# Performance work log

Hardware: AMD Instinct MI355X
Metric: run time of the kernel (lower is better)

## Reference

```python
import jax, jax.numpy as jnp
import numpy as np

N = 50000        # nodes
E = 800000       # edges
R = 8            # relations
G = 64           # g_dim
H1 = 64          # h1_dim
H2 = 32          # h2_dim (per-head for transformer, output for sage)
HEADS = 4
EPS = 1e-5       # BatchNorm eps


def setup_inputs() -> dict:
    key = jax.random.key(0)
    ks = jax.random.split(key, 16)
    def rn(k, shape, scale=0.05):
        return jax.random.normal(k, shape, dtype=jnp.float32) * scale
    return {
        "node_features": jax.random.normal(ks[0], (N, G), dtype=jnp.float32),
        "node_type": jax.random.randint(ks[1], (N,), 0, 3),
        "edge_index": jax.random.randint(ks[2], (2, E), 0, N),
        "edge_type": jax.random.randint(ks[3], (E,), 0, R),
        # RGCNConv params (per-relation weight + root weight + bias)
        "rgcn_w": rn(ks[4], (R, G, H1)),
        "rgcn_root": rn(ks[5], (G, H1)),
        "rgcn_bias": jnp.zeros((H1,), jnp.float32),
        "bn1_g": jnp.ones((H1,), jnp.float32),
        "bn1_b": jnp.zeros((H1,), jnp.float32),
        # TransformerConv params (q/k/v projections + skip)
        "wq": rn(ks[6], (H1, HEADS * H2)), "bq": jnp.zeros((HEADS * H2,), jnp.float32),
        "wk": rn(ks[7], (H1, HEADS * H2)), "bk": jnp.zeros((HEADS * H2,), jnp.float32),
        "wv": rn(ks[8], (H1, HEADS * H2)), "bv": jnp.zeros((HEADS * H2,), jnp.float32),
        "wskip": rn(ks[9], (H1, HEADS * H2)), "bskip": jnp.zeros((HEADS * H2,), jnp.float32),
        "bn2_g": jnp.ones((HEADS * H2,), jnp.float32),
        "bn2_b": jnp.zeros((HEADS * H2,), jnp.float32),
        # SAGEConv params (lin_l on aggregated neighbors has bias; lin_r on root has none)
        "sage_wl": rn(ks[10], (HEADS * H2, H2)), "sage_bl": jnp.zeros((H2,), jnp.float32),
        "sage_wr": rn(ks[11], (HEADS * H2, H2)),
        "bn3_g": jnp.ones((H2,), jnp.float32),
        "bn3_b": jnp.zeros((H2,), jnp.float32),
    }


def _bn(x, g, b):
    # BatchNorm1d in training mode: biased batch statistics over nodes
    m = x.mean(0)
    v = x.var(0)
    return g * (x - m) * jax.lax.rsqrt(v + EPS) + b


def _match(res, d):
    # F.pad(res, (0, d - c)): pads with zeros if d > c, truncates if d < c
    c = res.shape[1]
    if d > c:
        return jnp.pad(res, ((0, 0), (0, d - c)))
    return res[:, :d]


def _forward(node_features, rgcn_w, rgcn_root, rgcn_bias, bn1_g, bn1_b,
             wq, bq, wk, bk, wv, bv, wskip, bskip, bn2_g, bn2_b,
             sage_wl, sage_bl, sage_wr, bn3_g, bn3_b,
             edge_index, edge_type):
    src, dst = edge_index[0], edge_index[1]
    x = node_features
    residual = x

    # ---- RGCNConv: per-relation transform, per-relation mean aggregation, sum over relations ----
    xr = jnp.einsum('nf,rfh->nrh', x, rgcn_w)            # [N,R,H1]
    msg = xr[src, edge_type]                              # [E,H1]
    seg = dst * R + edge_type                             # segment per (node, relation)
    sums = jax.ops.segment_sum(msg, seg, num_segments=N * R)
    cnt = jax.ops.segment_sum(jnp.ones((E,), msg.dtype), seg, num_segments=N * R)
    agg = (sums / jnp.maximum(cnt, 1.0)[:, None]).reshape(N, R, H1).sum(1)
    h = agg + x @ rgcn_root + rgcn_bias
    h = jax.nn.leaky_relu(_bn(h, bn1_g, bn1_b))
    x = h + _match(residual, h.shape[1])
    residual = x

    # ---- TransformerConv: edge softmax attention, concat heads, + skip projection ----
    q = (x @ wq + bq).reshape(N, HEADS, H2)
    k = (x @ wk + bk).reshape(N, HEADS, H2)
    v = (x @ wv + bv).reshape(N, HEADS, H2)
    logits = (q[dst] * k[src]).sum(-1) / jnp.sqrt(jnp.float32(H2))  # [E,HEADS]
    mx = jax.ops.segment_max(logits, dst, num_segments=N)
    ex = jnp.exp(logits - mx[dst])
    den = jax.ops.segment_sum(ex, dst, num_segments=N)
    alpha = ex / jnp.maximum(den[dst], 1e-16)
    out = jax.ops.segment_sum(alpha[:, :, None] * v[src], dst, num_segments=N)
    h = out.reshape(N, HEADS * H2) + x @ wskip + bskip
    h = jax.nn.leaky_relu(_bn(h, bn2_g, bn2_b))
    x = h + _match(residual, h.shape[1])
    residual = x

    # ---- SAGEConv: mean neighbor aggregation + root transform ----
    nsum = jax.ops.segment_sum(x[src], dst, num_segments=N)
    ncnt = jax.ops.segment_sum(jnp.ones((E,), x.dtype), dst, num_segments=N)
    nmean = nsum / jnp.maximum(ncnt, 1.0)[:, None]
    h = nmean @ sage_wl + sage_bl + x @ sage_wr
    h = jax.nn.leaky_relu(_bn(h, bn3_g, bn3_b))
    return h + _match(residual, h.shape[1])


def reference(node_features, node_type, edge_index, edge_type,
              rgcn_w, rgcn_root, rgcn_bias, bn1_g, bn1_b,
              wq, bq, wk, bk, wv, bv, wskip, bskip, bn2_g, bn2_b,
              sage_wl, sage_bl, sage_wr, bn3_g, bn3_b):
    # node_type is unused by the original forward
    return _forward(node_features, rgcn_w, rgcn_root, rgcn_bias, bn1_g, bn1_b,
                    wq, bq, wk, bk, wv, bv, wskip, bskip, bn2_g, bn2_b,
                    sage_wl, sage_bl, sage_wr, bn3_g, bn3_b,
                    edge_index, edge_type)
```

## Files before the change

### kernel.cpp

```cpp
#include <hip/hip_runtime.h>
#include <stdint.h>

#define NN 50000
#define NE 800000
#define NR (NN*8)
#define SCAN_BS 512
#define NB2 782
#define INV_N (1.0f/50000.0f)
#define BN_EPS 1e-5f

typedef unsigned short ushort_t;
typedef unsigned char uchar_t;
typedef short bf16x8 __attribute__((ext_vector_type(8)));
typedef float f32x4 __attribute__((ext_vector_type(4)));
typedef float f32x2 __attribute__((ext_vector_type(2)));

__device__ __forceinline__ ushort_t f2bf(float f){
    unsigned int u = __float_as_uint(f);
    u += 0x7FFFu + ((u >> 16) & 1u);
    return (ushort_t)(u >> 16);
}
__device__ __forceinline__ float bf2f(ushort_t h){ return __uint_as_float(((unsigned int)h) << 16); }
__device__ __forceinline__ float bflo(unsigned int u){ return __uint_as_float(u << 16); }
__device__ __forceinline__ float bfhi(unsigned int u){ return __uint_as_float(u & 0xFFFF0000u); }

__device__ __forceinline__ unsigned int f4_to_fp8(float a, float b, float c, float d){
    int v = __builtin_amdgcn_cvt_pk_fp8_f32(a, b, 0, false);
    v = __builtin_amdgcn_cvt_pk_fp8_f32(c, d, v, true);
    return (unsigned int)v;
}
__device__ __forceinline__ void fp8_to_f4(unsigned int u, float& a, float& b, float& c, float& d){
    f32x2 lo = __builtin_amdgcn_cvt_pk_f32_fp8(u, false);
    f32x2 hi = __builtin_amdgcn_cvt_pk_f32_fp8(u, true);
    a = lo.x; b = lo.y; c = hi.x; d = hi.y;
}

__global__ void k_deg(const int* __restrict__ ei, const int* __restrict__ et,
                      int* __restrict__ deg, uint2* __restrict__ sr){
    int e = blockIdx.x*256 + threadIdx.x;
    if (e < NE){
        int seg = ei[NE + e]*8 + et[e];
        int rank = atomicAdd(&deg[seg], 1);
        uint2 o; o.x = (unsigned)seg; o.y = (unsigned)rank;
        sr[e] = o;
    }
}

__global__ void k_scan1(const int* __restrict__ deg, int* __restrict__ tmp, int* __restrict__ bsum){
    __shared__ int s[SCAN_BS];
    int t = threadIdx.x;
    int i = blockIdx.x*SCAN_BS + t;
    s[t] = (i < NR) ? deg[i] : 0;
    __syncthreads();
    for (int off = 1; off < SCAN_BS; off <<= 1){
        int add = (t >= off) ? s[t-off] : 0;
        __syncthreads();
        s[t] += add;
        __syncthreads();
    }
    if (i < NR) tmp[i] = s[t];
    if (t == SCAN_BS-1) bsum[blockIdx.x] = s[t];
}

__global__ void k_scan2(int* __restrict__ bsum){
    __shared__ int s[NB2];
    int t = threadIdx.x;
    if (t < NB2) s[t] = bsum[t];
    __syncthreads();
    if (t == 0){
        int acc = 0;
        for (int i = 0; i < NB2; ++i){ acc += s[i]; s[i] = acc; }
    }
    __syncthreads();
    if (t < NB2) bsum[t] = s[t];
}

__global__ void k_scan3(const int* __restrict__ tmp, const int* __restrict__ bsum, int* __restrict__ rs){
    int i = blockIdx.x*256 + threadIdx.x;
    if (i < NR){
        int b = i >> 9;
        int off = (b > 0) ? bsum[b-1] : 0;
        rs[i+1] = tmp[i] + off;
        if (i == 0) rs[0] = 0;
    }
}

__global__ void k_fill(const int* __restrict__ ei, const uint2* __restrict__ sr,
                       const int* __restrict__ rs, int* __restrict__ csr){
    int e = blockIdx.x*256 + threadIdx.x;
    if (e < NE){
        uint2 s = sr[e];
        csr[rs[s.x] + (int)s.y] = ei[e];
    }
}

__global__ void k_prep(const float* __restrict__ nf,
                       const float* __restrict__ rgcn_w, const float* __restrict__ root,
                       const float* __restrict__ wq, const float* __restrict__ wk,
                       const float* __restrict__ wv, const float* __restrict__ wsk,
                       const float* __restrict__ bq, const float* __restrict__ bk,
                       const float* __restrict__ bv, const float* __restrict__ bsk,
                       const float* __restrict__ wl, const float* __restrict__ wr,
                       ushort_t* __restrict__ xb, uchar_t* __restrict__ xb8,
                       ushort_t* __restrict__ Wcat,
                       ushort_t* __restrict__ Wt2, float* __restrict__ bcat,
                       ushort_t* __restrict__ Wsage){
    int i = blockIdx.x*256 + threadIdx.x;
    const int NXB = NN*16;
    if (i < NXB){
        float4 v = ((const float4*)nf)[i];
        ushort4 h;
        h.x = f2bf(v.x); h.y = f2bf(v.y); h.z = f2bf(v.z); h.w = f2bf(v.w);
        ((ushort4*)xb)[i] = h;
        ((unsigned int*)xb8)[i] = f4_to_fp8(v.x, v.y, v.z, v.w);
        return;
    }
    int j = i - NXB;
    if (j < 64*576){
        int h = j / 576, k = j - h*576;
        float v = (k < 512) ? rgcn_w[(size_t)k*64 + h] : root[(size_t)(k-512)*64 + h];
        Wcat[j] = f2bf(v);
    } else if (j < 64*576 + 512*64){
        int jj = j - 64*576;
        int c = jj >> 6, k = jj & 63;
        int mt = c >> 7, cc = c & 127;
        const float* W = (mt==0)?wq:(mt==1)?wk:(mt==2)?wv:wsk;
        Wt2[jj] = f2bf(W[(size_t)k*128 + cc]);
    } else if (j < 64*576 + 512*64 + 512){
        int c = j - (64*576 + 512*64);
        int mt = c >> 7, cc = c & 127;
        const float* B = (mt==0)?bq:(mt==1)?bk:(mt==2)?bv:bsk;
        bcat[c] = B[cc];
    } else if (j < 64*576 + 512*64 + 512 + 32*256){
        int jj = j - (64*576 + 512*64 + 512);
        int c = jj >> 8, k = jj & 255;
        float v = (k < 128) ? wr[(size_t)k*32 + c] : wl[(size_t)(k-128)*32 + c];
        Wsage[jj] = f2bf(v);
    }
}

__global__ __launch_bounds__(256) void rgcn_fused(const ushort_t* __restrict__ xb,
                                                  const uchar_t* __restrict__ xb8,
                                                  const int* __restrict__ rs,
                                                  const int* __restrict__ csr,
                                                  const ushort_t* __restrict__ Wcat,
                                                  const float* __restrict__ bias,
                                                  float* __restrict__ h1pre){
    __shared__ ushort_t Ml[16*520];
    int w = threadIdx.x >> 6, lane = threadIdx.x & 63;
    int quad = lane >> 4, l4 = lane & 15;
    int row0 = blockIdx.x * 16;
    int n0 = row0 + w*4;
    int rsel = (lane < 9 ? lane : 8);
    int rb = rs[n0*8 + rsel];
    int eb0 = __shfl(rb, 0);
    int dg0 = __shfl(rb, 8) - eb0;
    int idx = (lane < dg0) ? csr[eb0 + lane] : 0;
    for (int j = 0; j < 4; ++j){
        int lrow = (w*4 + j)*520;
        int ebase = __shfl(rb, 0);
        int enext = __shfl(rb, 8);
        int rb_next = 0, idxn = 0;
        if (j < 3){
            rb_next = rs[(n0 + j + 1)*8 + rsel];
            idxn = csr[min(enext + lane, NE - 1)];
        }
        int e0a = __shfl(rb, quad),     e1a = __shfl(rb, quad + 1);
        int e0b = __shfl(rb, quad + 4), e1b = __shfl(rb, quad + 5);
        int oa = e0a - ebase, la = e1a - e0a;
        int ob = e0b - ebase, lb = e1b - e0b;
        int ml = max(la, lb);
        ml = max(ml, __shfl_xor(ml, 16));
        ml = max(ml, __shfl_xor(ml, 32));
        float aa0=0.f, aa1=0.f, aa2=0.f, aa3=0.f;
        float ab0=0.f, ab1=0.f, ab2=0.f, ab3=0.f;
        for (int i = 0; i < ml; i += 4){
            int sA[4], sB[4];
            bool vA[4], vB[4];
#pragma unroll
            for (int u = 0; u < 4; ++u){
                int jA = oa + i + u, jB = ob + i + u;
                vA[u] = (i + u) < la;
                vB[u] = (i + u) < lb;
                int tA = __shfl(idx, jA & 63);
                int tB = __shfl(idx, jB & 63);
                if (jA >= 64 && vA[u]) tA = csr[ebase + jA];
                if (jB >= 64 && vB[u]) tB = csr[ebase + jB];
                sA[u] = vA[u] ? tA : 0;
                sB[u] = vB[u] ? tB : 0;
            }
            unsigned int uA[4], uB[4];
#pragma unroll
            for (int u = 0; u < 4; ++u){
                uA[u] = *(const unsigned int*)(xb8 + (size_t)sA[u]*64 + l4*4);
                uB[u] = *(const unsigned int*)(xb8 + (size_t)sB[u]*64 + l4*4);
            }
#pragma unroll
            for (int u = 0; u < 4; ++u){
                float f0,f1,f2,f3;
                fp8_to_f4(uA[u],f0,f1,f2,f3);
                if (vA[u]){ aa0+=f0; aa1+=f1; aa2+=f2; aa3+=f3; }
                fp8_to_f4(uB[u],f0,f1,f2,f3);
                if (vB[u]){ ab0+=f0; ab1+=f1; ab2+=f2; ab3+=f3; }
            }
        }
        float inva = 1.f / fmaxf((float)la, 1.f);
        float invb = 1.f / fmaxf((float)lb, 1.f);
        ushort4 oA, oB;
        oA.x = f2bf(aa0*inva); oA.y = f2bf(aa1*inva); oA.z = f2bf(aa2*inva); oA.w = f2bf(aa3*inva);
        oB.x = f2bf(ab0*invb); oB.y = f2bf(ab1*invb); oB.z = f2bf(ab2*invb); oB.w = f2bf(ab3*invb);
        *(ushort4*)&Ml[lrow + quad*64 + l4*4] = oA;
        *(ushort4*)&Ml[lrow + (quad + 4)*64 + l4*4] = oB;
        if (j < 3){
            rb = rb_next;
            int ebn = __shfl(rb, 0);
            int dgn = __shfl(rb, 8) - ebn;
            idx = (lane < dgn) ? idxn : 0;
        }
    }
    __syncthreads();
    int m = l4;
    f32x4 acc = {};
#pragma unroll
    for (int kt = 0; kt < 18; ++kt){
        int kk = kt*32 + quad*8;
        bf16x8 a;
        if (kt < 16) a = *(const bf16x8*)&Ml[m*520 + kk];
        else         a = *(const bf16x8*)(xb + (size_t)(row0 + m)*64 + (kk - 512));
        bf16x8 b = *(const bf16x8*)(Wcat + (size_t)(w*16 + m)*576 + kk);
        acc = __builtin_amdgcn_mfma_f32_16x16x32_bf16(a, b, acc, 0, 0, 0);
    }
    int col = w*16 + m;
    float bz = bias[col];
#pragma unroll
    for (int i = 0; i < 4; ++i){
        int rr = row0 + quad*4 + i;
        h1pre[(size_t)rr*64 + col] = acc[i] + bz;
    }
}

__global__ void bn1_finalize(const float* __restrict__ sums, const float* __restrict__ sumsq,
                             const float* __restrict__ g1, const float* __restrict__ b1,
                             float* __restrict__ A1, float* __restrict__ C1){
    int c = threadIdx.x;
    if (c < 64){
        float m = sums[c] * INV_N;
        float v = sumsq[c] * INV_N - m*m;
        float rsv = rsqrtf(fmaxf(v, 0.f) + BN_EPS);
        float A = rsv * g1[c];
        A1[c] = A;
        C1[c] = b1[c] - m * A;
    }
}

#define QS 132
#define BS 68
__global__ __launch_bounds__(256) void gemm_qkvs(const float* __restrict__ h1pre,
                                                 const float* __restrict__ nf,
                                                 const float* __restrict__ A1, const float* __restrict__ C1,
                                                 const ushort_t* __restrict__ Wt2,
                                                 const float* __restrict__ bcat,
                                                 ushort_t* __restrict__ qb,
                                                 uchar_t* __restrict__ kb8,
                                                 uchar_t* __restrict__ vb8,
                                                 ushort_t* __restrict__ sb){
    __shared__ ushort_t Bs[256*BS];
    __shared__ ushort_t pl[4][16*QS];
    int w = threadIdx.x >> 6, lane = threadIdx.x & 63;
    int m = lane & 15, quad = lane >> 4;
    int r0 = blockIdx.x*64 + w*16;
    int cg = blockIdx.y;
    int row = r0 + m;
    {
        int t = threadIdx.x;
        const ushort_t* wsrc = Wt2 + (size_t)cg*256*64;
#pragma unroll
        for (int u0 = 0; u0 < 8; ++u0){
            int u = u0*256 + t;
            int r = u >> 3, c8 = (u & 7)*8;
            *(uint4*)&Bs[r*BS + c8] = *(const uint4*)(wsrc + u*8);
        }
    }
    bf16x8 afrag[2];
#pragma unroll
    for (int kt = 0; kt < 2; ++kt){
        int db = kt*32 + quad*8;
        bf16x8 f = (bf16x8){0,0,0,0,0,0,0,0};
        if (row < NN){
            float4 h0 = *(const float4*)(h1pre + (size_t)row*64 + db);
            float4 h1 = *(const float4*)(h1pre + (size_t)row*64 + db + 4);
            float4 n0 = *(const float4*)(nf + (size_t)row*64 + db);
            float4 n1 = *(const float4*)(nf + (size_t)row*64 + db + 4);
            float4 a0 = *(const float4*)(A1 + db);
            float4 a1 = *(const float4*)(A1 + db + 4);
            float4 c0 = *(const float4*)(C1 + db);
            float4 c1 = *(const float4*)(C1 + db + 4);
            float hh[8] = {h0.x,h0.y,h0.z,h0.w,h1.x,h1.y,h1.z,h1.w};
            float nn[8] = {n0.x,n0.y,n0.z,n0.w,n1.x,n1.y,n1.z,n1.w};
            float AA[8] = {a0.x,a0.y,a0.z,a0.w,a1.x,a1.y,a1.z,a1.w};
            float CC[8] = {c0.x,c0.y,c0.z,c0.w,c1.x,c1.y,c1.z,c1.w};
#pragma unroll
            for (int e = 0; e < 8; ++e){
                float y = fmaf(hh[e], AA[e], CC[e]);
                y = (y >= 0.f) ? y : 0.01f*y;
                f[e] = (short)f2bf(y + nn[e]);
            }
        }
        afrag[kt] = f;
    }
    __syncthreads();
    f32x4 acc[16] = {};
#pragma unroll
    for (int kt = 0; kt < 2; ++kt){
        int kk = kt*32 + quad*8;
#pragma unroll
        for (int ct = 0; ct < 16; ++ct){
            bf16x8 b = *(const bf16x8*)&Bs[(size_t)(ct*16 + m)*BS + kk];
            acc[ct] = __builtin_amdgcn_mfma_f32_16x16x32_bf16(afrag[kt], b, acc[ct], 0, 0, 0);
        }
    }
#pragma unroll
    for (int ct = 0; ct < 8; ++ct){
        int g = cg*256 + ct*16 + m;
        float bz = bcat[g];
        int cc = g & 127;
#pragma unroll
        for (int i = 0; i < 4; ++i)
            pl[w][(quad*4 + i)*QS + cc] = f2bf(acc[ct][i] + bz);
    }
    if (cg == 0){
#pragma unroll
        for (int t = 0; t < 4; ++t){
            int u = t*64 + lane;
            int r = u >> 4, c = (u & 15)*8;
            int gr = r0 + r;
            if (gr < NN) *(uint4*)(qb + (size_t)gr*128 + c) = *(const uint4*)&pl[w][r*QS + c];
        }
    } else {
#pragma unroll
        for (int t = 0; t < 4; ++t){
            int u = t*64 + lane;
            int r = u >> 4, c = (u & 15)*8;
            int gr = r0 + r;
            if (gr < NN){
                uint4 vv4 = *(const uint4*)&pl[w][r*QS + c];
                uint2 o;
                o.x = f4_to_fp8(bflo(vv4.x), bfhi(vv4.x), bflo(vv4.y), bfhi(vv4.y));
                o.y = f4_to_fp8(bflo(vv4.z), bfhi(vv4.z), bflo(vv4.w), bfhi(vv4.w));
                *(uint2*)(vb8 + (size_t)gr*128 + c) = o;
            }
        }
    }
#pragma unroll
    for (int ct = 8; ct < 16; ++ct){
        int g = cg*256 + ct*16 + m;
        float bz = bcat[g];
        int cc = g & 127;
#pragma unroll
        for (int i = 0; i < 4; ++i)
            pl[w][(quad*4 + i)*QS + cc] = f2bf(acc[ct][i] + bz);
    }
    if (cg == 0){
#pragma unroll
        for (int t = 0; t < 4; ++t){
            int u = t*64 + lane;
            int r = u >> 4, c = (u & 15)*8;
            int gr = r0 + r;
            if (gr < NN){
                uint4 kk4 = *(const uint4*)&pl[w][r*QS + c];
                uint2 o;
                o.x = f4_to_fp8(bflo(kk4.x), bfhi(kk4.x), bflo(kk4.y), bfhi(kk4.y));
                o.y = f4_to_fp8(bflo(kk4.z), bfhi(kk4.z), bflo(kk4.w), bfhi(kk4.w));
                *(uint2*)(kb8 + (size_t)gr*128 + c) = o;
            }
        }
    } else {
#pragma unroll
        for (int t = 0; t < 4; ++t){
            int u = t*64 + lane;
            int r = u >> 4, c = (u & 15)*8;
            int gr = r0 + r;
            if (gr < NN) *(uint4*)(sb + (size_t)gr*128 + c) = *(const uint4*)&pl[w][r*QS + c];
        }
    }
}

__global__ __launch_bounds__(256) void sage_gemm(const ushort_t* __restrict__ x2b,
                                                 const ushort_t* __restrict__ nmeanb,
                                                 const ushort_t* __restrict__ Wsage,
                                                 const float* __restrict__ bl,
                                                 float* __restrict__ h3){
    int wv = threadIdx.x >> 6, lane = threadIdx.x & 63;
    int r0 = blockIdx.x*64 + wv*16;
    int m = lane & 15, quad = lane >> 4;
    int row = r0 + m;
    f32x4 acc[2] = {};
#pragma unroll
    for (int kt = 0; kt < 8; ++kt){
        int kk = kt*32 + quad*8;
        bf16x8 a;
        if (row < NN){
            const ushort_t* ap = (kt < 4) ? (x2b + (size_t)row*128 + kk)
                                          : (nmeanb + (size_t)row*128 + (kk - 128));
            a = *(const bf16x8*)ap;
        } else {
            a = (bf16x8){0,0,0,0,0,0,0,0};
        }
#pragma unroll
        for (int ct = 0; ct < 2; ++ct){
            bf16x8 b = *(const bf16x8*)(Wsage + (size_t)(ct*16 + m)*256 + kk);
            acc[ct] = __builtin_amdgcn_mfma_f32_16x16x32_bf16(a, b, acc[ct], 0, 0, 0);
        }
    }
#pragma unroll
    for (int ct = 0; ct < 2; ++ct){
        int col = ct*16 + m;
        float bz = bl[col];
#pragma unroll
        for (int i = 0; i < 4; ++i){
            int rr = r0 + quad*4 + i;
            if (rr < NN) h3[(size_t)rr*32 + col] = acc[ct][i] + bz;
        }
    }
}

template<int C>
__global__ __launch_bounds__(256) void bn_stats(const float* __restrict__ X, int ld,
                                                float* __restrict__ sums, float* __restrict__ sumsq){
    __shared__ float s1[256], s2[256];
    int t = threadIdx.x;
    int c = t & (C-1);
    const int rpb = 256 / C;
    int r = blockIdx.x * rpb + (t / C);
    int rstride = gridDim.x * rpb;
    float a = 0.f, b = 0.f;
    for (; r < NN; r += rstride){
        float v = X[(size_t)r*ld + c];
        a += v; b += v*v;
    }
    s1[t] = a; s2[t] = b;
    __syncthreads();
    for (int off = 128; off >= C; off >>= 1){
        if (t < off){ s1[t] += s1[t+off]; s2[t] += s2[t+off]; }
        __syncthreads();
    }
    if (t < C){ atomicAdd(&sums[t], s1[t]); atomicAdd(&sumsq[t], s2[t]); }
}

__device__ __forceinline__ float bn_leaky(float z, float m, float rsv, float g, float b){
    float y = (z - m) * rsv * g + b;
    return y >= 0.f ? y : 0.01f * y;
}

__global__ void bn_apply2(const float* __restrict__ h2, const float* __restrict__ h1pre,
                          const float* __restrict__ nf,
                          const float* __restrict__ g1, const float* __restrict__ b1,
                          const float* __restrict__ s1, const float* __restrict__ q1,
                          const float* __restrict__ g2, const float* __restrict__ b2,
                          const float* __restrict__ s2, const float* __restrict__ q2,
                          float* __restrict__ x2r, ushort_t* __restrict__ x2b,
                          uchar_t* __restrict__ x28){
    int i = blockIdx.x*256 + threadIdx.x;
    if (i >= NN*128) return;
    int n = i >> 7, c = i & 127;
    float m2 = s2[c] * INV_N;
    float v2 = q2[c] * INV_N - m2*m2;
    float rsv2 = rsqrtf(fmaxf(v2, 0.f) + BN_EPS);
    float val = bn_leaky(h2[i], m2, rsv2, g2[c], b2[c]);
    if (c < 64){
        float m1 = s1[c] * INV_N;
        float v1 = q1[c] * INV_N - m1*m1;
        float rsv1 = rsqrtf(fmaxf(v1, 0.f) + BN_EPS);
        val += bn_leaky(h1pre[(size_t)n*64 + c], m1, rsv1, g1[c], b1[c]) + nf[(size_t)n*64 + c];
    }
    if (c < 32) x2r[(size_t)n*32 + c] = val;
    x2b[i] = f2bf(val);
    int p = __builtin_amdgcn_cvt_pk_fp8_f32(val, val, 0, false);
    x28[i] = (uchar_t)(p & 0xFF);
}

__global__ void bn_apply3(const float* __restrict__ h3, const float* __restrict__ x2r,
                          const float* __restrict__ g, const float* __restrict__ b,
                          const float* __restrict__ sums, const float* __restrict__ sumsq,
                          float* __restrict__ out){
    int i = blockIdx.x*256 + threadIdx.x;
    if (i >= NN*32) return;
    int c = i & 31;
    float m = sums[c] * INV_N;
    float v = sumsq[c] * INV_N - m*m;
    float rsv = rsqrtf(fmaxf(v, 0.f) + BN_EPS);
    out[i] = bn_leaky(h3[i], m, rsv, g[c], b[c]) + x2r[i];
}

__global__ __launch_bounds__(256) void attn_kernel(const ushort_t* __restrict__ qb,
                                                   const uchar_t* __restrict__ kb8,
                                                   const uchar_t* __restrict__ vb8,
                                                   const ushort_t* __restrict__ sb,
                                                   const int* __restrict__ rs,
                                                   const int* __restrict__ csr,
                                                   float* __restrict__ h2){
    int w = threadIdx.x >> 6, lane = threadIdx.x & 63;
    int n = blockIdx.x*4 + w;
    if (n >= NN) return;
    int half = lane >> 5, l5 = lane & 31;
    int e0 = rs[n*8], e1 = rs[n*8 + 8];
    int deg = e1 - e0;
    uint2 qu = *(const uint2*)(qb + (size_t)n*128 + l5*4);
    uint2 sbv = *(const uint2*)(sb + (size_t)n*128 + l5*4);
    float q0 = bflo(qu.x), q1 = bfhi(qu.x), q2 = bflo(qu.y), q3 = bfhi(qu.y);
    const float scale = 0.17677669529663687f;
    int idx = 0;
    if (lane < deg) idx = csr[e0 + lane];
    int dcap = min(deg, 64);
    int nt = (dcap + 7) >> 3;
    float den = 0.f, a0 = 0.f, a1 = 0.f, a2 = 0.f, a3 = 0.f;
    for (int t = 0; t < nt; ++t){
        int i2 = t*8 + half*4;
        int j0 = i2, j1 = i2+1, j2 = i2+2, j3 = i2+3;
        bool v0 = j0 < dcap, v1 = j1 < dcap, v2 = j2 < dcap, v3 = j3 < dcap;
        int s0 = __shfl(idx, j0 & 63); s0 = v0 ? s0 : 0;
        int s1 = __shfl(idx, j1 & 63); s1 = v1 ? s1 : 0;
        int s2 = __shfl(idx, j2 & 63); s2 = v2 ? s2 : 0;
        int s3 = __shfl(idx, j3 & 63); s3 = v3 ? s3 : 0;
        unsigned int ku0 = *(const unsigned int*)(kb8 + (size_t)s0*128 + l5*4);
        unsigned int ku1 = *(const unsigned int*)(kb8 + (size_t)s1*128 + l5*4);
        unsigned int ku2 = *(const unsigned int*)(kb8 + (size_t)s2*128 + l5*4);
        unsigned int ku3 = *(const unsigned int*)(kb8 + (size_t)s3*128 + l5*4);
        unsigned int vu0 = *(const unsigned int*)(vb8 + (size_t)s0*128 + l5*4);
        unsigned int vu1 = *(const unsigned int*)(vb8 + (size_t)s1*128 + l5*4);
        unsigned int vu2 = *(const unsigned int*)(vb8 + (size_t)s2*128 + l5*4);
        unsigned int vu3 = *(const unsigned int*)(vb8 + (size_t)s3*128 + l5*4);
        float ka, kb_, kc, kd;
        fp8_to_f4(ku0, ka, kb_, kc, kd);
        float p0 = q0*ka + q1*kb_ + q2*kc + q3*kd;
        fp8_to_f4(ku1, ka, kb_, kc, kd);
        float p1 = q0*ka + q1*kb_ + q2*kc + q3*kd;
        fp8_to_f4(ku2, ka, kb_, kc, kd);
        float p2 = q0*ka + q1*kb_ + q2*kc + q3*kd;
        fp8_to_f4(ku3, ka, kb_, kc, kd);
        float p3 = q0*ka + q1*kb_ + q2*kc + q3*kd;
        p0 += __shfl_xor(p0, 1); p1 += __shfl_xor(p1, 1); p2 += __shfl_xor(p2, 1); p3 += __shfl_xor(p3, 1);
        p0 += __shfl_xor(p0, 2); p1 += __shfl_xor(p1, 2); p2 += __shfl_xor(p2, 2); p3 += __shfl_xor(p3, 2);
        p0 += __shfl_xor(p0, 4); p1 += __shfl_xor(p1, 4); p2 += __shfl_xor(p2, 4); p3 += __shfl_xor(p3, 4);
        float w0 = v0 ? __expf(p0 * scale) : 0.f;
        float w1 = v1 ? __expf(p1 * scale) : 0.f;
        float w2 = v2 ? __expf(p2 * scale) : 0.f;
        float w3 = v3 ? __expf(p3 * scale) : 0.f;
        den += w0 + w1 + w2 + w3;
        float va, vb_, vc, vd;
        fp8_to_f4(vu0, va, vb_, vc, vd);
        a0 = fmaf(w0, va, a0); a1 = fmaf(w0, vb_, a1); a2 = fmaf(w0, vc, a2); a3 = fmaf(w0, vd, a3);
        fp8_to_f4(vu1, va, vb_, vc, vd);
        a0 = fmaf(w1, va, a0); a1 = fmaf(w1, vb_, a1); a2 = fmaf(w1, vc, a2); a3 = fmaf(w1, vd, a3);
        fp8_to_f4(vu2, va, vb_, vc, vd);
        a0 = fmaf(w2, va, a0); a1 = fmaf(w2, vb_, a1); a2 = fmaf(w2, vc, a2); a3 = fmaf(w2, vd, a3);
        fp8_to_f4(vu3, va, vb_, vc, vd);
        a0 = fmaf(w3, va, a0); a1 = fmaf(w3, vb_, a1); a2 = fmaf(w3, vc, a2); a3 = fmaf(w3, vd, a3);
    }
    for (int e = 64 + half; e < deg; e += 2){
        int s = csr[e0 + e];
        unsigned int ku = *(const unsigned int*)(kb8 + (size_t)s*128 + l5*4);
        unsigned int vu = *(const unsigned int*)(vb8 + (size_t)s*128 + l5*4);
        float ka, kb_, kc, kd;
        fp8_to_f4(ku, ka, kb_, kc, kd);
        float p = q0*ka + q1*kb_ + q2*kc + q3*kd;
        p += __shfl_xor(p, 1);
        p += __shfl_xor(p, 2);
        p += __shfl_xor(p, 4);
        float wg = __expf(p * scale);
        den += wg;
        float va, vb_, vc, vd;
        fp8_to_f4(vu, va, vb_, vc, vd);
        a0 = fmaf(wg, va, a0); a1 = fmaf(wg, vb_, a1); a2 = fmaf(wg, vc, a2); a3 = fmaf(wg, vd, a3);
    }
    den += __shfl_xor(den, 32);
    a0 += __shfl_xor(a0, 32); a1 += __shfl_xor(a1, 32);
    a2 += __shfl_xor(a2, 32); a3 += __shfl_xor(a3, 32);
    if (half == 0){
        float inv = (den > 0.f) ? 1.f/den : 0.f;
        float4 o;
        o.x = bflo(sbv.x) + a0*inv;
        o.y = bfhi(sbv.x) + a1*inv;
        o.z = bflo(sbv.y) + a2*inv;
        o.w = bfhi(sbv.y) + a3*inv;
        *(float4*)(h2 + (size_t)n*128 + l5*4) = o;
    }
}

__global__ __launch_bounds__(256) void sage_agg(const uchar_t* __restrict__ x28,
                                                const int* __restrict__ rs,
                                                const int* __restrict__ csr,
                                                ushort_t* __restrict__ nmeanb){
    int w = threadIdx.x >> 6, lane = threadIdx.x & 63;
    int n = blockIdx.x*4 + w;
    if (n >= NN) return;
    int half = lane >> 5, l5 = lane & 31;
    int e0 = rs[n*8], e1 = rs[n*8 + 8];
    int deg = e1 - e0;
    int idx = 0;
    if (lane < deg) idx = csr[e0 + lane];
    int dcap = min(deg, 64);
    int nt = (dcap + 7) >> 3;
    float a0 = 0.f, a1 = 0.f, a2 = 0.f, a3 = 0.f;
    for (int t = 0; t < nt; ++t){
        int i2 = t*8 + half*4;
        int j0 = i2, j1 = i2+1, j2 = i2+2, j3 = i2+3;
        bool v0 = j0 < dcap, v1 = j1 < dcap, v2 = j2 < dcap, v3 = j3 < dcap;
        int s0 = __shfl(idx, j0 & 63); s0 = v0 ? s0 : 0;
        int s1 = __shfl(idx, j1 & 63); s1 = v1 ? s1 : 0;
        int s2 = __shfl(idx, j2 & 63); s2 = v2 ? s2 : 0;
        int s3 = __shfl(idx, j3 & 63); s3 = v3 ? s3 : 0;
        unsigned int u0 = *(const unsigned int*)(x28 + (size_t)s0*128 + l5*4);
        unsigned int u1 = *(const unsigned int*)(x28 + (size_t)s1*128 + l5*4);
        unsigned int u2 = *(const unsigned int*)(x28 + (size_t)s2*128 + l5*4);
        unsigned int u3 = *(const unsigned int*)(x28 + (size_t)s3*128 + l5*4);
        float fa, fb, fc, fd;
        if (v0){ fp8_to_f4(u0, fa, fb, fc, fd); a0 += fa; a1 += fb; a2 += fc; a3 += fd; }
        if (v1){ fp8_to_f4(u1, fa, fb, fc, fd); a0 += fa; a1 += fb; a2 += fc; a3 += fd; }
        if (v2){ fp8_to_f4(u2, fa, fb, fc, fd); a0 += fa; a1 += fb; a2 += fc; a3 += fd; }
        if (v3){ fp8_to_f4(u3, fa, fb, fc, fd); a0 += fa; a1 += fb; a2 += fc; a3 += fd; }
    }
    for (int e = 64 + half; e < deg; e += 2){
        int s = csr[e0 + e];
        unsigned int u = *(const unsigned int*)(x28 + (size_t)s*128 + l5*4);
        float fa, fb, fc, fd;
        fp8_to_f4(u, fa, fb, fc, fd);
        a0 += fa; a1 += fb; a2 += fc; a3 += fd;
    }
    a0 += __shfl_xor(a0, 32); a1 += __shfl_xor(a1, 32);
    a2 += __shfl_xor(a2, 32); a3 += __shfl_xor(a3, 32);
    if (half == 0){
        float inv = 1.f / fmaxf((float)deg, 1.f);
        ushort4 o;
        o.x = f2bf(a0*inv); o.y = f2bf(a1*inv); o.z = f2bf(a2*inv); o.w = f2bf(a3*inv);
        *(ushort4*)(nmeanb + (size_t)n*128 + l5*4) = o;
    }
}

extern "C" void kernel_launch(void* const* d_in, const int* in_sizes, int n_in,
                              void* d_out, int out_size, void* d_ws, size_t ws_size,
                              hipStream_t stream){
    const float* nf      = (const float*)d_in[0];
    const int*   ei      = (const int*)d_in[2];
    const int*   et      = (const int*)d_in[3];
    const float* rgcn_w  = (const float*)d_in[4];
    const float* root    = (const float*)d_in[5];
    const float* rbias   = (const float*)d_in[6];
    const float* bn1g    = (const float*)d_in[7];
    const float* bn1b    = (const float*)d_in[8];
    const float* wq      = (const float*)d_in[9];
    const float* bq      = (const float*)d_in[10];
    const float* wk      = (const float*)d_in[11];
    const float* bk      = (const float*)d_in[12];
    const float* wv      = (const float*)d_in[13];
    const float* bv      = (const float*)d_in[14];
    const float* wsk     = (const float*)d_in[15];
    const float* bsk     = (const float*)d_in[16];
    const float* bn2g    = (const float*)d_in[17];
    const float* bn2b    = (const float*)d_in[18];
    const float* wl      = (const float*)d_in[19];
    const float* bl      = (const float*)d_in[20];
    const float* wr      = (const float*)d_in[21];
    const float* bn3g    = (const float*)d_in[22];
    const float* bn3b    = (const float*)d_in[23];
    float* out = (float*)d_out;

    char* base = (char*)d_ws;
    size_t off = 0;
    auto take = [&](size_t bytes) -> char* {
        char* p = base + off;
        off += (bytes + 255) & ~(size_t)255;
        return p;
    };
    int*      deg    = (int*)take((size_t)NR*4);
    float*    bns    = (float*)take(1024*4);
    char*     zend   = base + off;
    int*      rs     = (int*)take((size_t)(NR+1)*4);
    int*      tmp    = (int*)take((size_t)NR*4);
    int*      bsum   = (int*)take(1024*4);
    uint2*    sr     = (uint2*)take((size_t)NE*8);
    int*      csr    = (int*)take((size_t)NE*4);
    ushort_t* Wcat   = (ushort_t*)take(64*576*2);
    ushort_t* Wt2    = (ushort_t*)take(512*64*2);
    float*    bcat   = (float*)take(512*4);
    ushort_t* Wsage  = (ushort_t*)take(32*256*2);
    ushort_t* xb     = (ushort_t*)take((size_t)NN*64*2);
    uchar_t*  xb8    = (uchar_t*)take((size_t)NN*64);
    float*    h1pre  = (float*)take((size_t)NN*64*4);
    float*    h2     = (float*)take((size_t)NN*128*4);
    float*    x2r    = (float*)take((size_t)NN*32*4);
    ushort_t* sb     = (ushort_t*)take((size_t)NN*128*2);
    char*     bigA   = take((size_t)NN*512*2);
    if (off > ws_size) return;

    ushort_t* qb     = (ushort_t*)(bigA + (size_t)NN*128);
    uchar_t*  vb8    = (uchar_t*)(bigA + (size_t)NN*384);
    uchar_t*  kb8    = (uchar_t*)(bigA + (size_t)NN*640);
    ushort_t* x2b    = (ushort_t*)bigA;
    uchar_t*  x28    = (uchar_t*)(bigA + (size_t)NN*256);
    ushort_t* nmeanb = (ushort_t*)(bigA + (size_t)NN*512);
    float*    h3     = (float*)(bigA + (size_t)NN*768);

    hipMemsetAsync(deg, 0, (size_t)(zend - (char*)deg), stream);

    const int PREP_N = NN*16 + 64*576 + 512*64 + 512 + 32*256;
    k_prep <<<(PREP_N+255)/256, 256, 0, stream>>>(nf, rgcn_w, root, wq, wk, wv, wsk,
                                                  bq, bk, bv, bsk, wl, wr,
                                                  xb, xb8, Wcat, Wt2, bcat, Wsage);
    k_deg  <<<(NE+255)/256, 256, 0, stream>>>(ei, et, deg, sr);
    k_scan1<<<NB2, SCAN_BS, 0, stream>>>(deg, tmp, bsum);
    k_scan2<<<1, 1024, 0, stream>>>(bsum);
    k_scan3<<<(NR+255)/256, 256, 0, stream>>>(tmp, bsum, rs);
    k_fill <<<(NE+255)/256, 256, 0, stream>>>(ei, sr, rs, csr);

    const int NB4 = (NN + 3) / 4;
    const int NBG = (NN + 63) / 64;

    rgcn_fused<<<NN/16, 256, 0, stream>>>(xb, xb8, rs, csr, Wcat, rbias, h1pre);
    bn_stats<64><<<256, 256, 0, stream>>>(h1pre, 64, bns + 0, bns + 64);
    bn1_finalize<<<1, 64, 0, stream>>>(bns + 0, bns + 64, bn1g, bn1b, bns + 448, bns + 512);

    gemm_qkvs<<<dim3(NBG, 2), 256, 0, stream>>>(h1pre, nf, bns + 448, bns + 512,
                                                Wt2, bcat, qb, kb8, vb8, sb);
    attn_kernel<<<NB4, 256, 0, stream>>>(qb, kb8, vb8, sb, rs, csr, h2);
    bn_stats<128><<<256, 256, 0, stream>>>(h2, 128, bns + 128, bns + 256);
    bn_apply2<<<(NN*128+255)/256, 256, 0, stream>>>(h2, h1pre, nf,
                                                    bn1g, bn1b, bns + 0, bns + 64,
                                                    bn2g, bn2b, bns + 128, bns + 256,
                                                    x2r, x2b, x28);

    sage_agg<<<NB4, 256, 0, stream>>>(x28, rs, csr, nmeanb);
    sage_gemm<<<NBG, 256, 0, stream>>>(x2b, nmeanb, Wsage, bl, h3);
    bn_stats<32><<<256, 256, 0, stream>>>(h3, 32, bns + 384, bns + 416);
    bn_apply3<<<(NN*32+255)/256, 256, 0, stream>>>(h3, x2r, bn3g, bn3b, bns + 384, bns + 416, out);
}
```

Before: 400.5 us.

## Fuse degree counting into prep, drop BN1 finalize, use packed fp8 accumulation

Folds the edge degree/rank atomic pass into the prep kernel and removes the separate bn1_finalize launch by computing the BN1 scale and shift inline in gemm_qkvs. It also swaps the serial scan2 for a parallel Hillis-Steele scan. The rgcn and sage gathers now accumulate with packed f32x2 fp8 conversions and masked loads instead of per-element branches, with spill edges beyond 64 handled in separate tail loops. The goal is fewer launches and cheaper inner loops, at the cost of redundant per-row BN arithmetic in the GEMM and wasted gathers of row 0 for masked lanes.

```diff
diff --git a/kernel.cpp b/kernel.cpp
--- a/kernel.cpp
+++ b/kernel.cpp
@@ -35,65 +35,6 @@
     a = lo.x; b = lo.y; c = hi.x; d = hi.y;
 }
 
-__global__ void k_deg(const int* __restrict__ ei, const int* __restrict__ et,
-                      int* __restrict__ deg, uint2* __restrict__ sr){
-    int e = blockIdx.x*256 + threadIdx.x;
-    if (e < NE){
-        int seg = ei[NE + e]*8 + et[e];
-        int rank = atomicAdd(&deg[seg], 1);
-        uint2 o; o.x = (unsigned)seg; o.y = (unsigned)rank;
-        sr[e] = o;
-    }
-}
-
-__global__ void k_scan1(const int* __restrict__ deg, int* __restrict__ tmp, int* __restrict__ bsum){
-    __shared__ int s[SCAN_BS];
-    int t = threadIdx.x;
-    int i = blockIdx.x*SCAN_BS + t;
-    s[t] = (i < NR) ? deg[i] : 0;
-    __syncthreads();
-    for (int off = 1; off < SCAN_BS; off <<= 1){
-        int add = (t >= off) ? s[t-off] : 0;
-        __syncthreads();
-        s[t] += add;
-        __syncthreads();
-    }
-    if (i < NR) tmp[i] = s[t];
-    if (t == SCAN_BS-1) bsum[blockIdx.x] = s[t];
-}
-
-__global__ void k_scan2(int* __restrict__ bsum){
-    __shared__ int s[NB2];
-    int t = threadIdx.x;
-    if (t < NB2) s[t] = bsum[t];
-    __syncthreads();
-    if (t == 0){
-        int acc = 0;
-        for (int i = 0; i < NB2; ++i){ acc += s[i]; s[i] = acc; }
-    }
-    __syncthreads();
-    if (t < NB2) bsum[t] = s[t];
-}
-
-__global__ void k_scan3(const int* __restrict__ tmp, const int* __restrict__ bsum, int* __restrict__ rs){
-    int i = blockIdx.x*256 + threadIdx.x;
-    if (i < NR){
-        int b = i >> 9;
-        int off = (b > 0) ? bsum[b-1] : 0;
-        rs[i+1] = tmp[i] + off;
-        if (i == 0) rs[0] = 0;
-    }
-}
-
-__global__ void k_fill(const int* __restrict__ ei, const uint2* __restrict__ sr,
-                       const int* __restrict__ rs, int* __restrict__ csr){
-    int e = blockIdx.x*256 + threadIdx.x;
-    if (e < NE){
-        uint2 s = sr[e];
-        csr[rs[s.x] + (int)s.y] = ei[e];
-    }
-}
-
 __global__ void k_prep(const float* __restrict__ nf,
                        const float* __restrict__ rgcn_w, const float* __restrict__ root,
                        const float* __restrict__ wq, const float* __restrict__ wk,
@@ -101,6 +42,8 @@
                        const float* __restrict__ bq, const float* __restrict__ bk,
                        const float* __restrict__ bv, const float* __restrict__ bsk,
                        const float* __restrict__ wl, const float* __restrict__ wr,
+                       const int* __restrict__ ei, const int* __restrict__ et,
+                       int* __restrict__ deg, uint2* __restrict__ sr,
                        ushort_t* __restrict__ xb, uchar_t* __restrict__ xb8,
                        ushort_t* __restrict__ Wcat,
                        ushort_t* __restrict__ Wt2, float* __restrict__ bcat,
@@ -136,6 +79,63 @@
         int c = jj >> 8, k = jj & 255;
         float v = (k < 128) ? wr[(size_t)k*32 + c] : wl[(size_t)(k-128)*32 + c];
         Wsage[jj] = f2bf(v);
+    } else {
+        int e = j - (64*576 + 512*64 + 512 + 32*256);
+        if (e < NE){
+            int seg = ei[NE + e]*8 + et[e];
+            int rank = atomicAdd(&deg[seg], 1);
+            uint2 o; o.x = (unsigned)seg; o.y = (unsigned)rank;
+            sr[e] = o;
+        }
+    }
+}
+
+__global__ void k_scan1(const int* __restrict__ deg, int* __restrict__ tmp, int* __restrict__ bsum){
+    __shared__ int s[SCAN_BS];
+    int t = threadIdx.x;
+    int i = blockIdx.x*SCAN_BS + t;
+    s[t] = (i < NR) ? deg[i] : 0;
+    __syncthreads();
+    for (int off = 1; off < SCAN_BS; off <<= 1){
+        int add = (t >= off) ? s[t-off] : 0;
+        __syncthreads();
+        s[t] += add;
+        __syncthreads();
+    }
+    if (i < NR) tmp[i] = s[t];
+    if (t == SCAN_BS-1) bsum[blockIdx.x] = s[t];
+}
+
+__global__ void k_scan2(int* __restrict__ bsum){
+    __shared__ int s[1024];
+    int t = threadIdx.x;
+    s[t] = (t < NB2) ? bsum[t] : 0;
+    __syncthreads();
+    for (int off = 1; off < 1024; off <<= 1){
+        int v = (t >= off) ? s[t-off] : 0;
+        __syncthreads();
+        s[t] += v;
+        __syncthreads();
+    }
+    if (t < NB2) bsum[t] = s[t];
+}
+
+__global__ void k_scan3(const int* __restrict__ tmp, const int* __restrict__ bsum, int* __restrict__ rs){
+    int i = blockIdx.x*256 + threadIdx.x;
+    if (i < NR){
+        int b = i >> 9;
+        int off = (b > 0) ? bsum[b-1] : 0;
+        rs[i+1] = tmp[i] + off;
+        if (i == 0) rs[0] = 0;
+    }
+}
+
+__global__ void k_fill(const int* __restrict__ ei, const uint2* __restrict__ sr,
+                       const int* __restrict__ rs, int* __restrict__ csr){
+    int e = blockIdx.x*256 + threadIdx.x;
+    if (e < NE){
+        uint2 s = sr[e];
+        csr[rs[s.x] + (int)s.y] = ei[e];
     }
 }
 
@@ -169,46 +169,52 @@
         int e0b = __shfl(rb, quad + 4), e1b = __shfl(rb, quad + 5);
         int oa = e0a - ebase, la = e1a - e0a;
         int ob = e0b - ebase, lb = e1b - e0b;
-        int ml = max(la, lb);
+        int laf = min(la, max(64 - oa, 0));
+        int lbf = min(lb, max(64 - ob, 0));
+        int ml = max(laf, lbf);
         ml = max(ml, __shfl_xor(ml, 16));
         ml = max(ml, __shfl_xor(ml, 32));
-        float aa0=0.f, aa1=0.f, aa2=0.f, aa3=0.f;
-        float ab0=0.f, ab1=0.f, ab2=0.f, ab3=0.f;
+        f32x2 aA0 = {0.f,0.f}, aA1 = {0.f,0.f};
+        f32x2 aB0 = {0.f,0.f}, aB1 = {0.f,0.f};
         for (int i = 0; i < ml; i += 4){
-            int sA[4], sB[4];
-            bool vA[4], vB[4];
+            unsigned int uA[4], uB[4];
 #pragma unroll
             for (int u = 0; u < 4; ++u){
                 int jA = oa + i + u, jB = ob + i + u;
-                vA[u] = (i + u) < la;
-                vB[u] = (i + u) < lb;
                 int tA = __shfl(idx, jA & 63);
                 int tB = __shfl(idx, jB & 63);
-                if (jA >= 64 && vA[u]) tA = csr[ebase + jA];
-                if (jB >= 64 && vB[u]) tB = csr[ebase + jB];
-                sA[u] = vA[u] ? tA : 0;
-                sB[u] = vB[u] ? tB : 0;
+                tA = ((i + u) < laf) ? tA : 0;
+                tB = ((i + u) < lbf) ? tB : 0;
+                uA[u] = *(const unsigned int*)(xb8 + (size_t)tA*64 + l4*4);
+                uB[u] = *(const unsigned int*)(xb8 + (size_t)tB*64 + l4*4);
             }
-            unsigned int uA[4], uB[4];
 #pragma unroll
             for (int u = 0; u < 4; ++u){
-                uA[u] = *(const unsigned int*)(xb8 + (size_t)sA[u]*64 + l4*4);
-                uB[u] = *(const unsigned int*)(xb8 + (size_t)sB[u]*64 + l4*4);
+                unsigned int a = ((i + u) < laf) ? uA[u] : 0u;
+                unsigned int b = ((i + u) < lbf) ? uB[u] : 0u;
+                aA0 += __builtin_amdgcn_cvt_pk_f32_fp8(a, false);
+                aA1 += __builtin_amdgcn_cvt_pk_f32_fp8(a, true);
+                aB0 += __builtin_amdgcn_cvt_pk_f32_fp8(b, false);
+                aB1 += __builtin_amdgcn_cvt_pk_f32_fp8(b, true);
             }
-#pragma unroll
-            for (int u = 0; u < 4; ++u){
-                float f0,f1,f2,f3;
-                fp8_to_f4(uA[u],f0,f1,f2,f3);
-                if (vA[u]){ aa0+=f0; aa1+=f1; aa2+=f2; aa3+=f3; }
-                fp8_to_f4(uB[u],f0,f1,f2,f3);
-                if (vB[u]){ ab0+=f0; ab1+=f1; ab2+=f2; ab3+=f3; }
-            }
+        }
+        for (int i = laf; i < la; ++i){
+            int t = csr[e0a + i];
+            unsigned int a = *(const unsigned int*)(xb8 + (size_t)t*64 + l4*4);
+            aA0 += __builtin_amdgcn_cvt_pk_f32_fp8(a, false);
+            aA1 += __builtin_amdgcn_cvt_pk_f32_fp8(a, true);
+        }
+        for (int i = lbf; i < lb; ++i){
+            int t = csr[e0b + i];
+            unsigned int b = *(const unsigned int*)(xb8 + (size_t)t*64 + l4*4);
+            aB0 += __builtin_amdgcn_cvt_pk_f32_fp8(b, false);
+            aB1 += __builtin_amdgcn_cvt_pk_f32_fp8(b, true);
         }
         float inva = 1.f / fmaxf((float)la, 1.f);
         float invb = 1.f / fmaxf((float)lb, 1.f);
         ushort4 oA, oB;
-        oA.x = f2bf(aa0*inva); oA.y = f2bf(aa1*inva); oA.z = f2bf(aa2*inva); oA.w = f2bf(aa3*inva);
-        oB.x = f2bf(ab0*invb); oB.y = f2bf(ab1*invb); oB.z = f2bf(ab2*invb); oB.w = f2bf(ab3*invb);
+        oA.x = f2bf(aA0.x*inva); oA.y = f2bf(aA0.y*inva); oA.z = f2bf(aA1.x*inva); oA.w = f2bf(aA1.y*inva);
+        oB.x = f2bf(aB0.x*invb); oB.y = f2bf(aB0.y*invb); oB.z = f2bf(aB1.x*invb); oB.w = f2bf(aB1.y*invb);
         *(ushort4*)&Ml[lrow + quad*64 + l4*4] = oA;
         *(ushort4*)&Ml[lrow + (quad + 4)*64 + l4*4] = oB;
         if (j < 3){
@@ -239,25 +245,12 @@
     }
 }
 
-__global__ void bn1_finalize(const float* __restrict__ sums, const float* __restrict__ sumsq,
-                             const float* __restrict__ g1, const float* __restrict__ b1,
-                             float* __restrict__ A1, float* __restrict__ C1){
-    int c = threadIdx.x;
-    if (c < 64){
-        float m = sums[c] * INV_N;
-        float v = sumsq[c] * INV_N - m*m;
-        float rsv = rsqrtf(fmaxf(v, 0.f) + BN_EPS);
-        float A = rsv * g1[c];
-        A1[c] = A;
-        C1[c] = b1[c] - m * A;
-    }
-}
-
 #define QS 132
 #define BS 68
 __global__ __launch_bounds__(256) void gemm_qkvs(const float* __restrict__ h1pre,
                                                  const float* __restrict__ nf,
-                                                 const float* __restrict__ A1, const float* __restrict__ C1,
+                                                 const float* __restrict__ s1, const float* __restrict__ q1,
+                                                 const float* __restrict__ g1, const float* __restrict__ b1,
                                                  const ushort_t* __restrict__ Wt2,
                                                  const float* __restrict__ bcat,
                                                  ushort_t* __restrict__ qb,
@@ -291,17 +284,27 @@
             float4 h1 = *(const float4*)(h1pre + (size_t)row*64 + db + 4);
             float4 n0 = *(const float4*)(nf + (size_t)row*64 + db);
             float4 n1 = *(const float4*)(nf + (size_t)row*64 + db + 4);
-            float4 a0 = *(const float4*)(A1 + db);
-            float4 a1 = *(const float4*)(A1 + db + 4);
-            float4 c0 = *(const float4*)(C1 + db);
-            float4 c1 = *(const float4*)(C1 + db + 4);
+            float4 sa = *(const float4*)(s1 + db);
+            float4 sb_ = *(const float4*)(s1 + db + 4);
+            float4 qa = *(const float4*)(q1 + db);
+            float4 qb_ = *(const float4*)(q1 + db + 4);
+            float4 ga = *(const float4*)(g1 + db);
+            float4 gb_ = *(const float4*)(g1 + db + 4);
+            float4 ba = *(const float4*)(b1 + db);
+            float4 bb_ = *(const float4*)(b1 + db + 4);
             float hh[8] = {h0.x,h0.y,h0.z,h0.w,h1.x,h1.y,h1.z,h1.w};
             float nn[8] = {n0.x,n0.y,n0.z,n0.w,n1.x,n1.y,n1.z,n1.w};
-            float AA[8] = {a0.x,a0.y,a0.z,a0.w,a1.x,a1.y,a1.z,a1.w};
-            float CC[8] = {c0.x,c0.y,c0.z,c0.w,c1.x,c1.y,c1.z,c1.w};
+            float SS[8] = {sa.x,sa.y,sa.z,sa.w,sb_.x,sb_.y,sb_.z,sb_.w};
+            float QQ[8] = {qa.x,qa.y,qa.z,qa.w,qb_.x,qb_.y,qb_.z,qb_.w};
+            float GG[8] = {ga.x,ga.y,ga.z,ga.w,gb_.x,gb_.y,gb_.z,gb_.w};
+            float BB[8] = {ba.x,ba.y,ba.z,ba.w,bb_.x,bb_.y,bb_.z,bb_.w};
 #pragma unroll
             for (int e = 0; e < 8; ++e){
-                float y = fmaf(hh[e], AA[e], CC[e]);
+                float mm = SS[e] * INV_N;
+                float vv = QQ[e] * INV_N - mm*mm;
+                float A = rsqrtf(fmaxf(vv, 0.f) + BN_EPS) * GG[e];
+                float C = BB[e] - mm * A;
+                float y = fmaf(hh[e], A, C);
                 y = (y >= 0.f) ? y : 0.01f*y;
                 f[e] = (short)f2bf(y + nn[e]);
             }
@@ -601,7 +604,7 @@
     if (lane < deg) idx = csr[e0 + lane];
     int dcap = min(deg, 64);
     int nt = (dcap + 7) >> 3;
-    float a0 = 0.f, a1 = 0.f, a2 = 0.f, a3 = 0.f;
+    f32x2 A0 = {0.f,0.f}, A1 = {0.f,0.f};
     for (int t = 0; t < nt; ++t){
         int i2 = t*8 + half*4;
         int j0 = i2, j1 = i2+1, j2 = i2+2, j3 = i2+3;
@@ -614,19 +617,24 @@
         unsigned int u1 = *(const unsigned int*)(x28 + (size_t)s1*128 + l5*4);
         unsigned int u2 = *(const unsigned int*)(x28 + (size_t)s2*128 + l5*4);
         unsigned int u3 = *(const unsigned int*)(x28 + (size_t)s3*128 + l5*4);
-        float fa, fb, fc, fd;
-        if (v0){ fp8_to_f4(u0, fa, fb, fc, fd); a0 += fa; a1 += fb; a2 += fc; a3 += fd; }
-        if (v1){ fp8_to_f4(u1, fa, fb, fc, fd); a0 += fa; a1 += fb; a2 += fc; a3 += fd; }
-        if (v2){ fp8_to_f4(u2, fa, fb, fc, fd); a0 += fa; a1 += fb; a2 += fc; a3 += fd; }
-        if (v3){ fp8_to_f4(u3, fa, fb, fc, fd); a0 += fa; a1 += fb; a2 += fc; a3 += fd; }
+        u0 = v0 ? u0 : 0u; u1 = v1 ? u1 : 0u;
+        u2 = v2 ? u2 : 0u; u3 = v3 ? u3 : 0u;
+        A0 += __builtin_amdgcn_cvt_pk_f32_fp8(u0, false);
+        A1 += __builtin_amdgcn_cvt_pk_f32_fp8(u0, true);
+        A0 += __builtin_amdgcn_cvt_pk_f32_fp8(u1, false);
+        A1 += __builtin_amdgcn_cvt_pk_f32_fp8(u1, true);
+        A0 += __builtin_amdgcn_cvt_pk_f32_fp8(u2, false);
+        A1 += __builtin_amdgcn_cvt_pk_f32_fp8(u2, true);
+        A0 += __builtin_amdgcn_cvt_pk_f32_fp8(u3, false);
+        A1 += __builtin_amdgcn_cvt_pk_f32_fp8(u3, true);
     }
     for (int e = 64 + half; e < deg; e += 2){
         int s = csr[e0 + e];
         unsigned int u = *(const unsigned int*)(x28 + (size_t)s*128 + l5*4);
-        float fa, fb, fc, fd;
-        fp8_to_f4(u, fa, fb, fc, fd);
-        a0 += fa; a1 += fb; a2 += fc; a3 += fd;
-    }
+        A0 += __builtin_amdgcn_cvt_pk_f32_fp8(u, false);
+        A1 += __builtin_amdgcn_cvt_pk_f32_fp8(u, true);
+    }
+    float a0 = A0.x, a1 = A0.y, a2 = A1.x, a3 = A1.y;
     a0 += __shfl_xor(a0, 32); a1 += __shfl_xor(a1, 32);
     a2 += __shfl_xor(a2, 32); a3 += __shfl_xor(a3, 32);
     if (half == 0){
@@ -703,11 +711,11 @@
 
     hipMemsetAsync(deg, 0, (size_t)(zend - (char*)deg), stream);
 
-    const int PREP_N = NN*16 + 64*576 + 512*64 + 512 + 32*256;
+    const int PREP_N = NN*16 + 64*576 + 512*64 + 512 + 32*256 + NE;
     k_prep <<<(PREP_N+255)/256, 256, 0, stream>>>(nf, rgcn_w, root, wq, wk, wv, wsk,
                                                   bq, bk, bv, bsk, wl, wr,
+                                                  ei, et, deg, sr,
                                                   xb, xb8, Wcat, Wt2, bcat, Wsage);
-    k_deg  <<<(NE+255)/256, 256, 0, stream>>>(ei, et, deg, sr);
     k_scan1<<<NB2, SCAN_BS, 0, stream>>>(deg, tmp, bsum);
     k_scan2<<<1, 1024, 0, stream>>>(bsum);
     k_scan3<<<(NR+255)/256, 256, 0, stream>>>(tmp, bsum, rs);
@@ -718,9 +726,8 @@
 
     rgcn_fused<<<NN/16, 256, 0, stream>>>(xb, xb8, rs, csr, Wcat, rbias, h1pre);
     bn_stats<64><<<256, 256, 0, stream>>>(h1pre, 64, bns + 0, bns + 64);
-    bn1_finalize<<<1, 64, 0, stream>>>(bns + 0, bns + 64, bn1g, bn1b, bns + 448, bns + 512);
-
-    gemm_qkvs<<<dim3(NBG, 2), 256, 0, stream>>>(h1pre, nf, bns + 448, bns + 512,
+
+    gemm_qkvs<<<dim3(NBG, 2), 256, 0, stream>>>(h1pre, nf, bns + 0, bns + 64, bn1g, bn1b,
                                                 Wt2, bcat, qb, kb8, vb8, sb);
     attn_kernel<<<NB4, 256, 0, stream>>>(qb, kb8, vb8, sb, rs, csr, h2);
     bn_stats<128><<<256, 256, 0, stream>>>(h2, 128, bns + 128, bns + 256);
```

After: 401.7 us. No clear change (+0.3%).
